# Kernel tuning notes

Hardware: AMD Instinct MI355X
Metric: run time of the kernel (lower is better)

Reference implementation:

```python
import jax, jax.numpy as jnp
import numpy as np

N_E = 1024
E_DIM = 256
BETA = 0.25
PERSISTENCE = 0.1
B, T = 16, 1024


def setup_inputs() -> dict:
    key = jax.random.key(0)
    k1, k2 = jax.random.split(key)
    z = jax.random.normal(k1, (B, T, E_DIM), dtype=jnp.float32)
    # nn.Embedding(1+n_e, e_dim) init uniform(-1/n_e, 1/n_e)
    emb_weight = jax.random.uniform(k2, (N_E + 1, E_DIM), dtype=jnp.float32,
                                    minval=-1.0 / N_E, maxval=1.0 / N_E)
    return {"z": z, "emb_weight": emb_weight}


def _loss_contrast(z, ind, book):
    # z: (B,T,e), ind: (B,T) int, book: (n_e+1, e)
    z_q = book[ind]                                   # (B,T,e)
    loss_indices = jnp.sum((z - z_q) ** 2, axis=-1)   # (B,T)
    # ||z - book||^2 expanded to avoid the (B,T,n_e+1,e) intermediate
    z_sq = jnp.sum(z * z, axis=-1)                    # (B,T)
    b_sq = jnp.sum(book * book, axis=-1)              # (n_e+1,)
    cross = jnp.einsum('bte,ne->btn', z, book)        # (B,T,n_e+1)
    loss_all = z_sq[..., None] + b_sq[None, None, :] - 2.0 * cross
    lc = jnp.maximum(loss_indices[..., None] - loss_all + 1e-6 / N_E, 0.0)
    return jnp.mean(lc)


def _forward(z, emb_weight):
    zf = z.reshape(-1, E_DIM)
    d = (jnp.sum(zf * zf, axis=1, keepdims=True)
         + jnp.sum(emb_weight * emb_weight, axis=1)
         - 2.0 * (zf @ emb_weight.T)).reshape(B, T, N_E + 1)

    ind0 = jnp.clip(jnp.argmin(d[:, 0, :], axis=1), 0, N_E - 1)  # (B,)

    def step(carry, d_t):
        ind, coe = carry                              # (B,) int, (B,) f32
        d_here = jnp.take_along_axis(d_t, ind[:, None], axis=1)[:, 0]
        ind_next = jnp.minimum(ind + 1, N_E - 1)
        d_next = jnp.take_along_axis(d_t, ind_next[:, None], axis=1)[:, 0]
        stay = d_here <= d_next - coe
        ind_new = jnp.where(stay, ind, ind_next)
        coe_new = jnp.where(stay, coe + PERSISTENCE / N_E, 0.0)
        return (ind_new, coe_new), ind_new

    coe0 = jnp.zeros((B,), jnp.float32)
    _, inds = jax.lax.scan(step, (ind0, coe0), jnp.swapaxes(d[:, 1:, :], 0, 1))
    encoding_indices = jnp.concatenate([ind0[None, :], inds], axis=0).T  # (B,T)

    book_sg = jax.lax.stop_gradient(emb_weight)  # torch uses .data/.detach() everywhere
    z_q_raw = book_sg[encoding_indices]
    z_q = z + jax.lax.stop_gradient(z_q_raw - z)  # straight-through

    # non-legacy: beta * L(z, sg(book)) + L(sg(z), sg(book))
    loss = (BETA * _loss_contrast(z, encoding_indices, book_sg)
            + _loss_contrast(jax.lax.stop_gradient(z), encoding_indices, book_sg))

    v = jnp.max(encoding_indices) - jnp.min(encoding_indices)
    return z_q, loss, encoding_indices, v


def reference(z, emb_weight):
    return _forward(z, emb_weight)
```

## Files before the change

### kernel.cpp

```cpp
#include <hip/hip_runtime.h>

#define N_E   1024
#define EDIM  256
#define BB    16
#define TT    1024
#define NROW  (BB*TT)
#define NCOL  1025
#define NPAD  1152
#define PERS  (0.1f/1024.0f)
#define EPSC  (1e-6f/1024.0f)

#define OUT_LOSS 4194304
#define OUT_IDX  4194305
#define OUT_V    4210689

#define WS_ZB   0ull
#define WS_BBF  8388608ull
#define WS_BSQ  8978432ull
#define WS_E    8983552ull
#define WS_IND  84481024ull
#define WS_PART 84546560ull

typedef __attribute__((ext_vector_type(8))) short short8;
typedef __attribute__((ext_vector_type(4))) float floatx4;

__device__ __forceinline__ unsigned short f2bf(float f) {
    unsigned int u = __float_as_uint(f);
    u = (u + 0x7fffu + ((u >> 16) & 1u)) >> 16;
    return (unsigned short)u;
}

__device__ __forceinline__ float gload_f32(const float* p) {
    float r;
    asm volatile("global_load_dword %0, %1, off" : "=v"(r) : "v"(p));
    return r;
}

__global__ __launch_bounds__(256) void k0_prep(const float* __restrict__ z,
                                               const float* __restrict__ book,
                                               unsigned short* __restrict__ zb,
                                               unsigned short* __restrict__ bb,
                                               float* __restrict__ bsq) {
    int bx = blockIdx.x, tid = threadIdx.x;
    if (bx < 4096) {
        float4 v = ((const float4*)z)[bx * 256 + tid];
        size_t o = ((size_t)bx * 256 + tid) * 4;
        zb[o + 0] = f2bf(v.x); zb[o + 1] = f2bf(v.y);
        zb[o + 2] = f2bf(v.z); zb[o + 3] = f2bf(v.w);
    } else {
        int row = bx - 4096;
        float v = (row < NCOL) ? book[(size_t)row * EDIM + tid] : 0.0f;
        bb[(size_t)row * EDIM + tid] = f2bf(v);
        __shared__ float sd[256];
        sd[tid] = v * v;
        __syncthreads();
        for (int s = 128; s > 0; s >>= 1) { if (tid < s) sd[tid] += sd[tid + s]; __syncthreads(); }
        if (tid == 0) bsq[row] = sd[0];
    }
}

__global__ __launch_bounds__(256) void k1_gemm(const unsigned short* __restrict__ zb,
                                               const unsigned short* __restrict__ bb,
                                               const float* __restrict__ bsq,
                                               float* __restrict__ e) {
    int tid = threadIdx.x;
    int lane = tid & 63, w = tid >> 6;
    int mBase = blockIdx.x * 128 + (w >> 1) * 64;
    int nBase = blockIdx.y * 128 + (w & 1) * 64;
    int r = lane & 15, q = lane >> 4;

    floatx4 acc[4][4];
    #pragma unroll
    for (int i = 0; i < 4; i++)
        #pragma unroll
        for (int j = 0; j < 4; j++) acc[i][j] = (floatx4){0.f, 0.f, 0.f, 0.f};

    const short8* A = (const short8*)zb;
    const short8* Bm = (const short8*)bb;

    #pragma unroll
    for (int ks = 0; ks < 8; ks++) {
        int k8 = ks * 4 + q;
        short8 a[4], b[4];
        #pragma unroll
        for (int i = 0; i < 4; i++) a[i] = A[(size_t)(mBase + i * 16 + r) * 32 + k8];
        #pragma unroll
        for (int j = 0; j < 4; j++) b[j] = Bm[(size_t)(nBase + j * 16 + r) * 32 + k8];
        #pragma unroll
        for (int i = 0; i < 4; i++)
            #pragma unroll
            for (int j = 0; j < 4; j++)
                acc[i][j] = __builtin_amdgcn_mfma_f32_16x16x32_bf16(a[i], b[j], acc[i][j], 0, 0, 0);
    }

    float bsql[4];
    #pragma unroll
    for (int j = 0; j < 4; j++) bsql[j] = bsq[nBase + j * 16 + r];

    #pragma unroll
    for (int i = 0; i < 4; i++)
        #pragma unroll
        for (int rr = 0; rr < 4; rr++) {
            int m = mBase + i * 16 + q * 4 + rr;
            float* erow = e + (size_t)m * NPAD;
            #pragma unroll
            for (int j = 0; j < 4; j++)
                erow[nBase + j * 16 + r] = fmaf(-2.0f, acc[i][j][rr], bsql[j]);
        }
}


#define DECLW float A0_0, A0_1, A0_2, A0_3, A0_4, A1_0, A1_1, A1_2, A1_3, A1_4; \
              int q_0, q_1, q_2, q_3, q_4;

#define LDOP(S,k) { int _t = _tb + 2*k + _g; _t = _t < 1024 ? _t : 1023; \
                    A##S##_##k = gload_f32(_pe + (size_t)_t * NPAD); }
#define LDSET(S) LDOP(S,0) LDOP(S,1) LDOP(S,2) LDOP(S,3) LDOP(S,4)

#define QCOP(S,k) { float _bv = __shfl_down(A##S##_##k, 1, 32); \
                    int _qv = (int)((_bv - A##S##_##k) * QS); \
                    q_##k = _capn ? 0 : _qv; }
#define QCSET(S) QCOP(S,0) QCOP(S,1) QCOP(S,2) QCOP(S,3) QCOP(S,4)

#define CHS(j,k,h) { int _rel = ind - cbc; \
                     int _qv = __builtin_amdgcn_readlane(q_##k, _rel + h); \
                     bool _stay = (kk <= _qv); \
                     int _ip1 = ind + 1; _ip1 = _ip1 < 1023 ? _ip1 : 1023; \
                     ind = _stay ? ind : _ip1; \
                     kk  = _stay ? kk + 1 : 0; \
                     packed = (lane == j) ? ind : packed; }
#define CHAIN CHS(0,0,0) CHS(1,0,32) CHS(2,1,0) CHS(3,1,32) CHS(4,2,0) \
              CHS(5,2,32) CHS(6,3,0) CHS(7,3,32) CHS(8,4,0) CHS(9,4,32)

#define ITERX(SI, SQ) { \
    int cbI = ind < 992 ? ind : 992;                  \
    { const float* _pe = eb + cbI + _cl; int _tb = t + 20; LDSET(SI) } \
    __builtin_amdgcn_sched_barrier(0); \
    int packed = 0; \
    CHAIN \
    if (lane < 10 && t + lane < 1024) wind[ibase + t + lane] = packed; \
    __builtin_amdgcn_sched_barrier(0); \
    asm volatile("s_waitcnt vmcnt(6)" ::: "memory");  \
    __builtin_amdgcn_sched_barrier(0); \
    { bool _capn = (cbn + _cl == 1023); QCSET(SQ) } \
    cbc = cbn; cbn = cbI; \
    t += 10; }

__global__ __launch_bounds__(256, 1) void k2_scan(const float* __restrict__ z,
                                                  const float* __restrict__ book,
                                                  const float* __restrict__ bsq,
                                                  const float* __restrict__ e,
                                                  int* __restrict__ wind) {
    __shared__ float sb[4]; __shared__ int si[4];

    int b = blockIdx.x, tid = threadIdx.x;
    int lane = tid & 63, w = tid >> 6;

    const float4* zr = (const float4*)(z + (size_t)b * TT * EDIM);
    float4 zv = zr[lane];
    float s = zv.x * zv.x + zv.y * zv.y + zv.z * zv.z + zv.w * zv.w;
    #pragma unroll
    for (int off = 32; off; off >>= 1) s += __shfl_xor(s, off, 64);
    float zsq = s;

    float best = 3.4e38f; int bidx = 0;
    for (int wi = w; wi < 17; wi += 4) {
        int n = wi * 64 + lane;
        if (n < NCOL) {
            const float4* br = (const float4*)(book + (size_t)n * EDIM);
            float c0 = 0.f, c1 = 0.f, c2 = 0.f, c3 = 0.f;
            #pragma unroll 8
            for (int k = 0; k < 64; k++) {
                float4 bo = br[k]; float4 za = zr[k];
                c0 = fmaf(za.x, bo.x, c0); c1 = fmaf(za.y, bo.y, c1);
                c2 = fmaf(za.z, bo.z, c2); c3 = fmaf(za.w, bo.w, c3);
            }
            float cr = (c0 + c1) + (c2 + c3);
            float d0 = (zsq + bsq[n]) - 2.0f * cr;
            if (d0 < best || (d0 == best && n < bidx)) { best = d0; bidx = n; }
        }
    }
    #pragma unroll
    for (int off = 32; off; off >>= 1) {
        float ob = __shfl_xor(best, off, 64);
        int   oi = __shfl_xor(bidx, off, 64);
        if (ob < best || (ob == best && oi < bidx)) { best = ob; bidx = oi; }
    }
    if (lane == 0) { sb[w] = best; si[w] = bidx; }
    __syncthreads();
    if (w != 0) return;

    best = sb[0]; bidx = si[0];
    for (int i = 1; i < 4; i++) {
        float vv = sb[i]; int ii = si[i];
        if (vv < best || (vv == best && ii < bidx)) { best = vv; bidx = ii; }
    }

    int ind = min(bidx, N_E - 1);
    int kk = 0;
    size_t ibase = (size_t)b * TT;
    if (lane == 0) wind[ibase] = ind;

    const float* eb = e + (size_t)b * TT * NPAD;
    const float QS = 1.0f / PERS;

    int _g = lane >> 5;
    int _cl = lane & 31;

    DECLW

    int cbc = ind < 992 ? ind : 992;
    int cbn = cbc;
    { const float* _pe = eb + cbc + _cl; int _tb = 1;  LDSET(0) }
    { const float* _pe = eb + cbn + _cl; int _tb = 11; LDSET(1) }
    asm volatile("s_waitcnt vmcnt(5)" ::: "memory");
    __builtin_amdgcn_sched_barrier(0);
    { bool _capn = (cbc + _cl == 1023); QCSET(0) }

    int t = 1;
    #pragma unroll 1
    for (int cc = 0; cc < 52; cc++) {
        ITERX(0, 1)
        ITERX(1, 0)
    }
}

__global__ __launch_bounds__(256) void k3_loss_zq(const float* __restrict__ e,
                                                  const int* __restrict__ wind,
                                                  const float* __restrict__ book,
                                                  float* __restrict__ part,
                                                  float* __restrict__ out) {
    int rIdx = blockIdx.x, tid = threadIdx.x;
    int ind = wind[rIdx];
    const float* er = e + (size_t)rIdx * NPAD;
    float eind = er[ind];
    float p = 0.0f;
    for (int n = tid; n < NCOL; n += 256) {
        float v = eind - er[n] + EPSC;
        p += v > 0.0f ? v : 0.0f;
    }
    __shared__ float sd[256];
    sd[tid] = p; __syncthreads();
    for (int s = 128; s > 0; s >>= 1) { if (tid < s) sd[tid] += sd[tid + s]; __syncthreads(); }
    if (tid == 0) { part[rIdx] = sd[0]; out[OUT_IDX + rIdx] = (float)ind; }
    out[(size_t)rIdx * 256 + tid] = book[(size_t)ind * EDIM + tid];
}

__global__ __launch_bounds__(256) void k4_final(const float* __restrict__ part,
                                                const int* __restrict__ wind,
                                                float* __restrict__ out) {
    int tid = threadIdx.x;
    float s = 0.0f;
    for (int i = tid; i < NROW; i += 256) s += part[i];
    __shared__ float sd[256];
    sd[tid] = s; __syncthreads();
    for (int st = 128; st > 0; st >>= 1) { if (tid < st) sd[tid] += sd[tid + st]; __syncthreads(); }
    if (tid == 0) {
        int mn = wind[0], mx = wind[TT - 1];
        for (int b = 1; b < BB; b++) {
            mn = min(mn, wind[(size_t)b * TT]);
            mx = max(mx, wind[(size_t)b * TT + TT - 1]);
        }
        out[OUT_LOSS] = 1.25f * sd[0] / ((float)NROW * (float)NCOL);
        out[OUT_V] = (float)(mx - mn);
    }
}

extern "C" void kernel_launch(void* const* d_in, const int* in_sizes, int n_in,
                              void* d_out, int out_size, void* d_ws, size_t ws_size,
                              hipStream_t stream) {
    const float* z    = (const float*)d_in[0];
    const float* book = (const float*)d_in[1];
    char* ws = (char*)d_ws;
    unsigned short* zb = (unsigned short*)(ws + WS_ZB);
    unsigned short* bb = (unsigned short*)(ws + WS_BBF);
    float* bsq  = (float*)(ws + WS_BSQ);
    float* e    = (float*)(ws + WS_E);
    int*   wind = (int*)(ws + WS_IND);
    float* part = (float*)(ws + WS_PART);
    float* out  = (float*)d_out;

    hipLaunchKernelGGL(k0_prep,    dim3(4096 + 1152), dim3(256), 0, stream, z, book, zb, bb, bsq);
    hipLaunchKernelGGL(k1_gemm,    dim3(128, 9),      dim3(256), 0, stream, zb, bb, bsq, e);
    hipLaunchKernelGGL(k2_scan,    dim3(16),          dim3(256), 0, stream, z, book, bsq, e, wind);
    hipLaunchKernelGGL(k3_loss_zq, dim3(16384),       dim3(256), 0, stream, e, wind, book, part, out);
    hipLaunchKernelGGL(k4_final,   dim3(1),           dim3(256), 0, stream, part, wind, out);
}
```

Measured before the change: 241.0 us.

## Deepen scan prefetch pipeline to four stages of six timesteps each

Restructures the sequential index-chain scan so global loads of distance windows run four stages ahead in chunks of six timesteps, instead of two stages of ten. The aim is to hide more global-memory latency behind the serial dependency chain. Each chunk is now shorter, so base indices are looked up more often, and the vmcnt bookkeeping and the volatile dummy stores have to stay consistent for correctness.

```diff
diff --git a/kernel.cpp b/kernel.cpp
--- a/kernel.cpp
+++ b/kernel.cpp
@@ -110,41 +110,50 @@
 }
 
 
-#define DECLW float A0_0, A0_1, A0_2, A0_3, A0_4, A1_0, A1_1, A1_2, A1_3, A1_4; \
-              int q_0, q_1, q_2, q_3, q_4;
-
-#define LDOP(S,k) { int _t = _tb + 2*k + _g; _t = _t < 1024 ? _t : 1023; \
+#define GCH 6
+
+#define DECLW float A0_0, A0_1, A0_2, A1_0, A1_1, A1_2, \
+                    A2_0, A2_1, A2_2, A3_0, A3_1, A3_2; \
+              int q_0, q_1, q_2;
+
+#define LDOP(S,k) { int _t = ti + 2*k + _g; _t = _t < 1024 ? _t : 1023; \
                     A##S##_##k = gload_f32(_pe + (size_t)_t * NPAD); }
-#define LDSET(S) LDOP(S,0) LDOP(S,1) LDOP(S,2) LDOP(S,3) LDOP(S,4)
+#define LDSET0 LDOP(0,0) LDOP(0,1) LDOP(0,2)
+#define LDSET1 LDOP(1,0) LDOP(1,1) LDOP(1,2)
+#define LDSET2 LDOP(2,0) LDOP(2,1) LDOP(2,2)
+#define LDSET3 LDOP(3,0) LDOP(3,1) LDOP(3,2)
 
 #define QCOP(S,k) { float _bv = __shfl_down(A##S##_##k, 1, 32); \
                     int _qv = (int)((_bv - A##S##_##k) * QS); \
                     q_##k = _capn ? 0 : _qv; }
-#define QCSET(S) QCOP(S,0) QCOP(S,1) QCOP(S,2) QCOP(S,3) QCOP(S,4)
-
-#define CHS(j,k,h) { int _rel = ind - cbc; \
+#define QCSET0 QCOP(0,0) QCOP(0,1) QCOP(0,2)
+#define QCSET1 QCOP(1,0) QCOP(1,1) QCOP(1,2)
+#define QCSET2 QCOP(2,0) QCOP(2,1) QCOP(2,2)
+#define QCSET3 QCOP(3,0) QCOP(3,1) QCOP(3,2)
+
+#define CHS(j,k,h) { int _rel = ind - b0; \
                      int _qv = __builtin_amdgcn_readlane(q_##k, _rel + h); \
                      bool _stay = (kk <= _qv); \
                      int _ip1 = ind + 1; _ip1 = _ip1 < 1023 ? _ip1 : 1023; \
                      ind = _stay ? ind : _ip1; \
                      kk  = _stay ? kk + 1 : 0; \
                      packed = (lane == j) ? ind : packed; }
-#define CHAIN CHS(0,0,0) CHS(1,0,32) CHS(2,1,0) CHS(3,1,32) CHS(4,2,0) \
-              CHS(5,2,32) CHS(6,3,0) CHS(7,3,32) CHS(8,4,0) CHS(9,4,32)
+#define CHAIN6 CHS(0,0,0) CHS(1,0,32) CHS(2,1,0) CHS(3,1,32) CHS(4,2,0) CHS(5,2,32)
 
 #define ITERX(SI, SQ) { \
     int cbI = ind < 992 ? ind : 992;                  \
-    { const float* _pe = eb + cbI + _cl; int _tb = t + 20; LDSET(SI) } \
+    { const float* _pe = eb + cbI + _cl; int ti = t + 24; LDSET##SI } \
     __builtin_amdgcn_sched_barrier(0); \
     int packed = 0; \
-    CHAIN \
-    if (lane < 10 && t + lane < 1024) wind[ibase + t + lane] = packed; \
+    CHAIN6 \
+    if (lane < GCH && t + lane < 1024) wind[ibase + t + lane] = packed; \
     __builtin_amdgcn_sched_barrier(0); \
-    asm volatile("s_waitcnt vmcnt(6)" ::: "memory");  \
+    asm volatile("s_waitcnt vmcnt(13)" ::: "memory");  \
     __builtin_amdgcn_sched_barrier(0); \
-    { bool _capn = (cbn + _cl == 1023); QCSET(SQ) } \
-    cbc = cbn; cbn = cbI; \
-    t += 10; }
+    { bool _capn = (b1 + _cl == 1023); QCSET##SQ } \
+    __builtin_amdgcn_sched_barrier(0); \
+    b0 = b1; b1 = b2; b2 = b3; b3 = cbI; \
+    t += GCH; }
 
 __global__ __launch_bounds__(256, 1) void k2_scan(const float* __restrict__ z,
                                                   const float* __restrict__ book,
@@ -199,7 +208,6 @@
     int ind = min(bidx, N_E - 1);
     int kk = 0;
     size_t ibase = (size_t)b * TT;
-    if (lane == 0) wind[ibase] = ind;
 
     const float* eb = e + (size_t)b * TT * NPAD;
     const float QS = 1.0f / PERS;
@@ -209,19 +217,36 @@
 
     DECLW
 
-    int cbc = ind < 992 ? ind : 992;
-    int cbn = cbc;
-    { const float* _pe = eb + cbc + _cl; int _tb = 1;  LDSET(0) }
-    { const float* _pe = eb + cbn + _cl; int _tb = 11; LDSET(1) }
-    asm volatile("s_waitcnt vmcnt(5)" ::: "memory");
+    asm volatile("s_waitcnt vmcnt(0)" ::: "memory");
     __builtin_amdgcn_sched_barrier(0);
-    { bool _capn = (cbc + _cl == 1023); QCSET(0) }
+
+    int base0 = ind < 992 ? ind : 992;
+    int b0 = base0, b1 = base0, b2 = base0, b3 = base0;
+
+    { const float* _pe = eb + base0 + _cl; int ti = 1;  LDSET0 }
+    if (lane == 0) *(volatile int*)(wind + ibase) = ind;
+    { const float* _pe = eb + base0 + _cl; int ti = 7;  LDSET1 }
+    if (lane == 0) *(volatile int*)(wind + ibase) = ind;
+    { const float* _pe = eb + base0 + _cl; int ti = 13; LDSET2 }
+    if (lane == 0) *(volatile int*)(wind + ibase) = ind;
+    { const float* _pe = eb + base0 + _cl; int ti = 19; LDSET3 }
+    if (lane == 0) *(volatile int*)(wind + ibase) = ind;
+    __builtin_amdgcn_sched_barrier(0);
+    asm volatile("s_waitcnt vmcnt(13)" ::: "memory");
+    __builtin_amdgcn_sched_barrier(0);
+    {
+        bool _capn = (b0 + _cl == 1023);
+        QCSET0
+    }
+    __builtin_amdgcn_sched_barrier(0);
 
     int t = 1;
     #pragma unroll 1
-    for (int cc = 0; cc < 52; cc++) {
+    for (int cc = 0; cc < 43; cc++) {
         ITERX(0, 1)
-        ITERX(1, 0)
+        ITERX(1, 2)
+        ITERX(2, 3)
+        ITERX(3, 0)
     }
 }
 
```

New measurement: 241.0 us. No clear change (+0.0%).

## Split scan into producer warps filling LDS ring and single consumer chain warp

Applied to the files above, without the earlier changes.

The sequential index scan now runs in a 512-thread block where seven producer wavefronts load 64-wide windows of the distance matrix for 6 timesteps, quantize neighbor differences, and publish them to a shared-memory ring. The single consumer wavefront only reads the ring and advances the chain, then tells the producers the next window base with a lookahead of 4 chunks. The goal is to take global-load latency off the serial critical path. In exchange it adds spin-wait flag synchronization through LDS, and the window must stay valid despite the lookahead base (window widened to 64, base cap 960).

```diff
diff --git a/kernel.cpp b/kernel.cpp
--- a/kernel.cpp
+++ b/kernel.cpp
@@ -110,51 +110,32 @@
 }
 
 
-#define DECLW float A0_0, A0_1, A0_2, A0_3, A0_4, A1_0, A1_1, A1_2, A1_3, A1_4; \
-              int q_0, q_1, q_2, q_3, q_4;
-
-#define LDOP(S,k) { int _t = _tb + 2*k + _g; _t = _t < 1024 ? _t : 1023; \
-                    A##S##_##k = gload_f32(_pe + (size_t)_t * NPAD); }
-#define LDSET(S) LDOP(S,0) LDOP(S,1) LDOP(S,2) LDOP(S,3) LDOP(S,4)
-
-#define QCOP(S,k) { float _bv = __shfl_down(A##S##_##k, 1, 32); \
-                    int _qv = (int)((_bv - A##S##_##k) * QS); \
-                    q_##k = _capn ? 0 : _qv; }
-#define QCSET(S) QCOP(S,0) QCOP(S,1) QCOP(S,2) QCOP(S,3) QCOP(S,4)
-
-#define CHS(j,k,h) { int _rel = ind - cbc; \
-                     int _qv = __builtin_amdgcn_readlane(q_##k, _rel + h); \
-                     bool _stay = (kk <= _qv); \
-                     int _ip1 = ind + 1; _ip1 = _ip1 < 1023 ? _ip1 : 1023; \
-                     ind = _stay ? ind : _ip1; \
-                     kk  = _stay ? kk + 1 : 0; \
-                     packed = (lane == j) ? ind : packed; }
-#define CHAIN CHS(0,0,0) CHS(1,0,32) CHS(2,1,0) CHS(3,1,32) CHS(4,2,0) \
-              CHS(5,2,32) CHS(6,3,0) CHS(7,3,32) CHS(8,4,0) CHS(9,4,32)
-
-#define ITERX(SI, SQ) { \
-    int cbI = ind < 992 ? ind : 992;                  \
-    { const float* _pe = eb + cbI + _cl; int _tb = t + 20; LDSET(SI) } \
-    __builtin_amdgcn_sched_barrier(0); \
-    int packed = 0; \
-    CHAIN \
-    if (lane < 10 && t + lane < 1024) wind[ibase + t + lane] = packed; \
-    __builtin_amdgcn_sched_barrier(0); \
-    asm volatile("s_waitcnt vmcnt(6)" ::: "memory");  \
-    __builtin_amdgcn_sched_barrier(0); \
-    { bool _capn = (cbn + _cl == 1023); QCSET(SQ) } \
-    cbc = cbn; cbn = cbI; \
-    t += 10; }
-
-__global__ __launch_bounds__(256, 1) void k2_scan(const float* __restrict__ z,
+#define NCH 171
+#define DLA 4
+
+#define CHS1(j) { int _rel = ind - b0; \
+    int _qv = __builtin_amdgcn_readlane(q_##j, _rel); \
+    bool _stay = (kk <= _qv); \
+    int _ip1 = ind + 1; _ip1 = _ip1 < 1023 ? _ip1 : 1023; \
+    ind = _stay ? ind : _ip1; \
+    kk  = _stay ? kk + 1 : 0; \
+    packed = (lane == j) ? ind : packed; }
+
+__global__ __launch_bounds__(512, 1) void k2_scan(const float* __restrict__ z,
                                                   const float* __restrict__ book,
                                                   const float* __restrict__ bsq,
                                                   const float* __restrict__ e,
                                                   int* __restrict__ wind) {
-    __shared__ float sb[4]; __shared__ int si[4];
+    __shared__ float sb[8]; __shared__ int si[8];
+    __shared__ int ringq[8][6][64];
+    __shared__ int dflag[8];
+    __shared__ int sready[8];
+    __shared__ int sbase[8];
 
     int b = blockIdx.x, tid = threadIdx.x;
     int lane = tid & 63, w = tid >> 6;
+
+    if (tid < 8) { dflag[tid] = -1; sready[tid] = -1; }
 
     const float4* zr = (const float4*)(z + (size_t)b * TT * EDIM);
     float4 zv = zr[lane];
@@ -164,7 +145,7 @@
     float zsq = s;
 
     float best = 3.4e38f; int bidx = 0;
-    for (int wi = w; wi < 17; wi += 4) {
+    for (int wi = w; wi < 17; wi += 8) {
         int n = wi * 64 + lane;
         if (n < NCOL) {
             const float4* br = (const float4*)(book + (size_t)n * EDIM);
@@ -188,10 +169,42 @@
     }
     if (lane == 0) { sb[w] = best; si[w] = bidx; }
     __syncthreads();
-    if (w != 0) return;
+
+    const float* eb = e + (size_t)b * TT * NPAD;
+    const float QS = 1.0f / PERS;
+
+    if (w != 0) {
+        for (int c = w - 1; c < NCH; c += 7) {
+            int slot = c & 7;
+            while (*(volatile int*)&sready[slot] != c) {}
+            asm volatile("" ::: "memory");
+            int base = *(volatile int*)&sbase[slot];
+            int t0 = 1 + 6 * c;
+            const float* pw = eb + base + lane;
+            float A_0, A_1, A_2, A_3, A_4, A_5;
+            { int tr = t0 + 0; tr = tr < 1024 ? tr : 1023; A_0 = gload_f32(pw + (size_t)tr * NPAD); }
+            { int tr = t0 + 1; tr = tr < 1024 ? tr : 1023; A_1 = gload_f32(pw + (size_t)tr * NPAD); }
+            { int tr = t0 + 2; tr = tr < 1024 ? tr : 1023; A_2 = gload_f32(pw + (size_t)tr * NPAD); }
+            { int tr = t0 + 3; tr = tr < 1024 ? tr : 1023; A_3 = gload_f32(pw + (size_t)tr * NPAD); }
+            { int tr = t0 + 4; tr = tr < 1024 ? tr : 1023; A_4 = gload_f32(pw + (size_t)tr * NPAD); }
+            { int tr = t0 + 5; tr = tr < 1024 ? tr : 1023; A_5 = gload_f32(pw + (size_t)tr * NPAD); }
+            asm volatile("s_waitcnt vmcnt(0)" ::: "memory");
+            __builtin_amdgcn_sched_barrier(0);
+            bool cap = (base + lane == 1023);
+            ringq[slot][0][lane] = cap ? 0 : (int)((__shfl_down(A_0, 1, 64) - A_0) * QS);
+            ringq[slot][1][lane] = cap ? 0 : (int)((__shfl_down(A_1, 1, 64) - A_1) * QS);
+            ringq[slot][2][lane] = cap ? 0 : (int)((__shfl_down(A_2, 1, 64) - A_2) * QS);
+            ringq[slot][3][lane] = cap ? 0 : (int)((__shfl_down(A_3, 1, 64) - A_3) * QS);
+            ringq[slot][4][lane] = cap ? 0 : (int)((__shfl_down(A_4, 1, 64) - A_4) * QS);
+            ringq[slot][5][lane] = cap ? 0 : (int)((__shfl_down(A_5, 1, 64) - A_5) * QS);
+            asm volatile("s_waitcnt lgkmcnt(0)" ::: "memory");
+            if (lane == 0) *(volatile int*)&dflag[slot] = c;
+        }
+        return;
+    }
 
     best = sb[0]; bidx = si[0];
-    for (int i = 1; i < 4; i++) {
+    for (int i = 1; i < 8; i++) {
         float vv = sb[i]; int ii = si[i];
         if (vv < best || (vv == best && ii < bidx)) { best = vv; bidx = ii; }
     }
@@ -201,27 +214,47 @@
     size_t ibase = (size_t)b * TT;
     if (lane == 0) wind[ibase] = ind;
 
-    const float* eb = e + (size_t)b * TT * NPAD;
-    const float QS = 1.0f / PERS;
-
-    int _g = lane >> 5;
-    int _cl = lane & 31;
-
-    DECLW
-
-    int cbc = ind < 992 ? ind : 992;
-    int cbn = cbc;
-    { const float* _pe = eb + cbc + _cl; int _tb = 1;  LDSET(0) }
-    { const float* _pe = eb + cbn + _cl; int _tb = 11; LDSET(1) }
-    asm volatile("s_waitcnt vmcnt(5)" ::: "memory");
-    __builtin_amdgcn_sched_barrier(0);
-    { bool _capn = (cbc + _cl == 1023); QCSET(0) }
+    int B0 = ind < 960 ? ind : 960;
+    int b0 = B0, b1 = B0, b2 = B0, b3 = B0;
+
+    if (lane == 0) { sbase[0] = B0; sbase[1] = B0; sbase[2] = B0; sbase[3] = B0; }
+    asm volatile("s_waitcnt lgkmcnt(0)" ::: "memory");
+    if (lane == 0) {
+        *(volatile int*)&sready[0] = 0;
+        *(volatile int*)&sready[1] = 1;
+        *(volatile int*)&sready[2] = 2;
+        *(volatile int*)&sready[3] = 3;
+    }
 
     int t = 1;
     #pragma unroll 1
-    for (int cc = 0; cc < 52; cc++) {
-        ITERX(0, 1)
-        ITERX(1, 0)
+    for (int c = 0; c < NCH; c++) {
+        int slot = c & 7;
+        while (*(volatile int*)&dflag[slot] != c) {}
+        asm volatile("" ::: "memory");
+        int q_0 = ringq[slot][0][lane];
+        int q_1 = ringq[slot][1][lane];
+        int q_2 = ringq[slot][2][lane];
+        int q_3 = ringq[slot][3][lane];
+        int q_4 = ringq[slot][4][lane];
+        int q_5 = ringq[slot][5][lane];
+
+        int packed = 0;
+        CHS1(0) CHS1(1) CHS1(2) CHS1(3) CHS1(4) CHS1(5)
+        if (lane < 6 && t + lane < 1024) wind[ibase + t + lane] = packed;
+
+        int nc = c + DLA;
+        if (nc < NCH) {
+            int nb = ind < 960 ? ind : 960;
+            int ns = nc & 7;
+            if (lane == 0) sbase[ns] = nb;
+            asm volatile("s_waitcnt lgkmcnt(0)" ::: "memory");
+            if (lane == 0) *(volatile int*)&sready[ns] = nc;
+            b0 = b1; b1 = b2; b2 = b3; b3 = nb;
+        } else {
+            b0 = b1; b1 = b2; b2 = b3;
+        }
+        t += 6;
     }
 }
 
@@ -282,7 +315,7 @@
 
     hipLaunchKernelGGL(k0_prep,    dim3(4096 + 1152), dim3(256), 0, stream, z, book, zb, bb, bsq);
     hipLaunchKernelGGL(k1_gemm,    dim3(128, 9),      dim3(256), 0, stream, zb, bb, bsq, e);
-    hipLaunchKernelGGL(k2_scan,    dim3(16),          dim3(256), 0, stream, z, book, bsq, e, wind);
+    hipLaunchKernelGGL(k2_scan,    dim3(16),          dim3(512), 0, stream, z, book, bsq, e, wind);
     hipLaunchKernelGGL(k3_loss_zq, dim3(16384),       dim3(256), 0, stream, e, wind, book, part, out);
     hipLaunchKernelGGL(k4_final,   dim3(1),           dim3(256), 0, stream, part, wind, out);
 }
```

After: 262.5 us. 8.9% more time.

## Recompute distance tiles in loss kernel instead of rereading stored distance matrix

Applied to the files above, without the earlier changes.

The loss kernel no longer reads the 16384x1152 fp32 distance matrix. It recomputes distance tiles with bf16 MFMA from the prepped z and codebook. It first recomputes the chunks covering each row's chosen index to get the selected distance, then runs a second full pass to accumulate the hinge loss, and it also writes z_q and the indices. This trades roughly 75 MB of memory reads for recomputing the GEMM on only 128 blocks, which risks low occupancy and extra compute; the first GEMM kernel still writes the matrix for the scan.

```diff
diff --git a/kernel.cpp b/kernel.cpp
--- a/kernel.cpp
+++ b/kernel.cpp
@@ -109,7 +109,6 @@
         }
 }
 
-
 #define DECLW float A0_0, A0_1, A0_2, A0_3, A0_4, A1_0, A1_1, A1_2, A1_3, A1_4; \
               int q_0, q_1, q_2, q_3, q_4;
 
@@ -225,33 +224,129 @@
     }
 }
 
-__global__ __launch_bounds__(256) void k3_loss_zq(const float* __restrict__ e,
-                                                  const int* __restrict__ wind,
-                                                  const float* __restrict__ book,
-                                                  float* __restrict__ part,
-                                                  float* __restrict__ out) {
-    int rIdx = blockIdx.x, tid = threadIdx.x;
-    int ind = wind[rIdx];
-    const float* er = e + (size_t)rIdx * NPAD;
-    float eind = er[ind];
-    float p = 0.0f;
-    for (int n = tid; n < NCOL; n += 256) {
-        float v = eind - er[n] + EPSC;
-        p += v > 0.0f ? v : 0.0f;
-    }
+__global__ __launch_bounds__(256) void k3_fused(const unsigned short* __restrict__ zb,
+                                                const unsigned short* __restrict__ bb,
+                                                const float* __restrict__ bsq,
+                                                const int* __restrict__ wind,
+                                                const float* __restrict__ book,
+                                                float* __restrict__ part,
+                                                float* __restrict__ out) {
+    int tid = threadIdx.x;
+    int lane = tid & 63, w = tid >> 6;
+    int r = lane & 15, q = lane >> 4;
+    int mB = blockIdx.x * 128;
+    int mBase = mB + (w >> 1) * 64;
+    int rowW = (w >> 1) * 64;
+
+    __shared__ int   sind[128];
+    __shared__ float seind[128];
     __shared__ float sd[256];
-    sd[tid] = p; __syncthreads();
+
+    if (tid < 128) sind[tid] = wind[mB + tid];
+    __syncthreads();
+
+    int ca = sind[0] >> 7, cb2 = sind[127] >> 7;
+
+    const short8* A = (const short8*)zb;
+    const short8* Bm = (const short8*)bb;
+
+    for (int ch = ca; ch <= cb2; ch++) {
+        int nBase = ch * 128 + (w & 1) * 64;
+        floatx4 acc[4][4];
+        #pragma unroll
+        for (int i = 0; i < 4; i++)
+            #pragma unroll
+            for (int j = 0; j < 4; j++) acc[i][j] = (floatx4){0.f, 0.f, 0.f, 0.f};
+        #pragma unroll
+        for (int ks = 0; ks < 8; ks++) {
+            int k8 = ks * 4 + q;
+            short8 a[4], b[4];
+            #pragma unroll
+            for (int i = 0; i < 4; i++) a[i] = A[(size_t)(mBase + i * 16 + r) * 32 + k8];
+            #pragma unroll
+            for (int j = 0; j < 4; j++) b[j] = Bm[(size_t)(nBase + j * 16 + r) * 32 + k8];
+            #pragma unroll
+            for (int i = 0; i < 4; i++)
+                #pragma unroll
+                for (int j = 0; j < 4; j++)
+                    acc[i][j] = __builtin_amdgcn_mfma_f32_16x16x32_bf16(a[i], b[j], acc[i][j], 0, 0, 0);
+        }
+        float bsql[4];
+        #pragma unroll
+        for (int j = 0; j < 4; j++) bsql[j] = bsq[nBase + j * 16 + r];
+        #pragma unroll
+        for (int i = 0; i < 4; i++)
+            #pragma unroll
+            for (int rr = 0; rr < 4; rr++) {
+                int rowl = rowW + i * 16 + q * 4 + rr;
+                int indr = sind[rowl];
+                #pragma unroll
+                for (int j = 0; j < 4; j++) {
+                    int col = nBase + j * 16 + r;
+                    if (col == indr) seind[rowl] = fmaf(-2.0f, acc[i][j][rr], bsql[j]);
+                }
+            }
+    }
+    __syncthreads();
+
+    float psum = 0.0f;
+    for (int ch = 0; ch < 9; ch++) {
+        int nBase = ch * 128 + (w & 1) * 64;
+        floatx4 acc[4][4];
+        #pragma unroll
+        for (int i = 0; i < 4; i++)
+            #pragma unroll
+            for (int j = 0; j < 4; j++) acc[i][j] = (floatx4){0.f, 0.f, 0.f, 0.f};
+        #pragma unroll
+        for (int ks = 0; ks < 8; ks++) {
+            int k8 = ks * 4 + q;
+            short8 a[4], b[4];
+            #pragma unroll
+            for (int i = 0; i < 4; i++) a[i] = A[(size_t)(mBase + i * 16 + r) * 32 + k8];
+            #pragma unroll
+            for (int j = 0; j < 4; j++) b[j] = Bm[(size_t)(nBase + j * 16 + r) * 32 + k8];
+            #pragma unroll
+            for (int i = 0; i < 4; i++)
+                #pragma unroll
+                for (int j = 0; j < 4; j++)
+                    acc[i][j] = __builtin_amdgcn_mfma_f32_16x16x32_bf16(a[i], b[j], acc[i][j], 0, 0, 0);
+        }
+        float bsql[4];
+        #pragma unroll
+        for (int j = 0; j < 4; j++) bsql[j] = bsq[nBase + j * 16 + r];
+        #pragma unroll
+        for (int i = 0; i < 4; i++)
+            #pragma unroll
+            for (int rr = 0; rr < 4; rr++) {
+                int rowl = rowW + i * 16 + q * 4 + rr;
+                float ei = seind[rowl];
+                #pragma unroll
+                for (int j = 0; j < 4; j++) {
+                    int col = nBase + j * 16 + r;
+                    if (col <= 1024) {
+                        float v = ei - fmaf(-2.0f, acc[i][j][rr], bsql[j]) + EPSC;
+                        psum += v > 0.0f ? v : 0.0f;
+                    }
+                }
+            }
+    }
+    sd[tid] = psum; __syncthreads();
     for (int s = 128; s > 0; s >>= 1) { if (tid < s) sd[tid] += sd[tid + s]; __syncthreads(); }
-    if (tid == 0) { part[rIdx] = sd[0]; out[OUT_IDX + rIdx] = (float)ind; }
-    out[(size_t)rIdx * 256 + tid] = book[(size_t)ind * EDIM + tid];
+    if (tid == 0) part[blockIdx.x] = sd[0];
+
+    if (tid < 128) out[OUT_IDX + mB + tid] = (float)sind[tid];
+    #pragma unroll 4
+    for (int rr = 0; rr < 128; rr++) {
+        int ind = sind[rr];
+        out[(size_t)(mB + rr) * 256 + tid] = book[(size_t)ind * EDIM + tid];
+    }
 }
 
 __global__ __launch_bounds__(256) void k4_final(const float* __restrict__ part,
                                                 const int* __restrict__ wind,
                                                 float* __restrict__ out) {
     int tid = threadIdx.x;
-    float s = 0.0f;
-    for (int i = tid; i < NROW; i += 256) s += part[i];
+    float s = (tid < 128) ? part[tid] : 0.0f;
     __shared__ float sd[256];
     sd[tid] = s; __syncthreads();
     for (int st = 128; st > 0; st >>= 1) { if (tid < st) sd[tid] += sd[tid + st]; __syncthreads(); }
@@ -280,9 +375,9 @@
     float* part = (float*)(ws + WS_PART);
     float* out  = (float*)d_out;
 
-    hipLaunchKernelGGL(k0_prep,    dim3(4096 + 1152), dim3(256), 0, stream, z, book, zb, bb, bsq);
-    hipLaunchKernelGGL(k1_gemm,    dim3(128, 9),      dim3(256), 0, stream, zb, bb, bsq, e);
-    hipLaunchKernelGGL(k2_scan,    dim3(16),          dim3(256), 0, stream, z, book, bsq, e, wind);
-    hipLaunchKernelGGL(k3_loss_zq, dim3(16384),       dim3(256), 0, stream, e, wind, book, part, out);
-    hipLaunchKernelGGL(k4_final,   dim3(1),           dim3(256), 0, stream, part, wind, out);
-}
+    hipLaunchKernelGGL(k0_prep,   dim3(4096 + 1152), dim3(256), 0, stream, z, book, zb, bb, bsq);
+    hipLaunchKernelGGL(k1_gemm,   dim3(128, 9),      dim3(256), 0, stream, zb, bb, bsq, e);
+    hipLaunchKernelGGL(k2_scan,   dim3(16),          dim3(256), 0, stream, z, book, bsq, e, wind);
+    hipLaunchKernelGGL(k3_fused,  dim3(128),         dim3(256), 0, stream, zb, bb, bsq, wind, book, part, out);
+    hipLaunchKernelGGL(k4_final,  dim3(1),           dim3(256), 0, stream, part, wind, out);
+}
```

Result: slower. 262.8 us (+9.1%).
